# Kernel tuning notes

Measured on AMD Instinct MI355X. Metric: run time of the kernel, lower is better.

## Reference

```python
import jax, jax.numpy as jnp
import numpy as np

B, N, M = 4, 8192, 8192


def setup_inputs() -> dict:
    key = jax.random.key(0)
    k1, k2, k3, k4 = jax.random.split(key, 4)
    xyz1 = jax.random.normal(k1, (B, N, 3), dtype=jnp.float32)
    xyz2 = jax.random.normal(k2, (B, M, 3), dtype=jnp.float32)
    weights1 = jax.random.uniform(k3, (B, N), dtype=jnp.float32)
    weights2 = jax.random.uniform(k4, (B, M), dtype=jnp.float32)
    return {"xyz1": xyz1, "xyz2": xyz2, "weights1": weights1, "weights2": weights2}


def _chamfer_dists(xyz1, xyz2):
    # Squared L2 pairwise distances via the ||a||^2 + ||b||^2 - 2 a.b identity
    # (avoids materializing a [B, N, M, 3] difference tensor).
    sq1 = jnp.sum(xyz1 * xyz1, axis=-1)            # [B, N]
    sq2 = jnp.sum(xyz2 * xyz2, axis=-1)            # [B, M]
    dots = jnp.einsum("bnc,bmc->bnm", xyz1, xyz2)  # [B, N, M]
    d = sq1[:, :, None] + sq2[:, None, :] - 2.0 * dots
    d = jnp.maximum(d, 0.0)
    dist1 = jnp.min(d, axis=2)  # [B, N] nearest in xyz2 for each point in xyz1
    dist2 = jnp.min(d, axis=1)  # [B, M] nearest in xyz1 for each point in xyz2
    return dist1, dist2


def reference(xyz1, xyz2, weights1, weights2):
    dist1, dist2 = _chamfer_dists(xyz1, xyz2)
    dist1 = dist1 * weights1
    dist2 = dist2 * weights2
    dist1_avg = jnp.sum(dist1) / jnp.sum(weights1)
    dist2_avg = jnp.sum(dist2) / jnp.sum(weights2)
    return (dist1_avg + dist2_avg) / 2.0
```

## Files before the change

kernel.cpp:

```cpp
#include <hip/hip_runtime.h>

#define TPB 256
constexpr int Bsz  = 4;
constexpr int Npts = 8192;
constexpr int Mpts = 8192;
constexpr int PTS  = Bsz * Npts;
constexpr int QT_PER_B = Npts / 16;
constexpr int CT_PER_B = Mpts / 16;
constexpr int RBLK = 64;

typedef __attribute__((ext_vector_type(8))) short short8;
typedef __attribute__((ext_vector_type(4))) float f32x4;

__device__ __forceinline__ float min3f(float a, float b, float c) {
    return fminf(fminf(a, b), c);
}

__device__ __forceinline__ unsigned short bfh(float v) {
    unsigned u = __float_as_uint(v);
    return (unsigned short)((u + 0x7fffu + ((u >> 16) & 1u)) >> 16);
}
__device__ __forceinline__ float b2f(unsigned short h) {
    return __uint_as_float(((unsigned)h) << 16);
}
__device__ __forceinline__ void split3(float v, unsigned short& h,
                                       unsigned short& m, unsigned short& l) {
    h = bfh(v); float fh = b2f(h);
    m = bfh(v - fh); float fm = b2f(m);
    l = bfh(v - fh - fm);
}

__device__ __forceinline__ unsigned short pickA(int o, unsigned short h,
                                                unsigned short m, unsigned short l) {
    return o < 3 ? h : (o < 5 ? m : l);
}
__device__ __forceinline__ unsigned short pickB(int o, unsigned short h,
                                                unsigned short m, unsigned short l) {
    return (o == 1 || o == 4) ? m : (o == 2 ? l : h);
}

__global__ void __launch_bounds__(TPB) prep_kernel(
    const float* __restrict__ xyz1, const float* __restrict__ xyz2,
    short* __restrict__ aQ, short* __restrict__ bC)
{
    int id   = blockIdx.x * TPB + threadIdx.x;
    int side = id >> 17;
    int tl   = id & 131071;
    int tile = tl >> 6, lane = tl & 63;
    int r = lane & 15, g = lane >> 4;

    const float* src = side ? xyz2 : xyz1;
    int p = tile * 16 + r;
    float x = src[p * 3 + 0], y = src[p * 3 + 1], z = src[p * 3 + 2];
    float n = fmaf(x, x, fmaf(y, y, z * z));
    float s = side ? 1.f : -2.f;

    unsigned short xh, xm, xl, yh, ym, yl, zh, zm, zl, nh, nm, nl;
    split3(s * x, xh, xm, xl);
    split3(s * y, yh, ym, yl);
    split3(s * z, zh, zm, zl);
    split3(n, nh, nm, nl);
    const unsigned short ONE = 0x3F80;

    short8 v;
#pragma unroll
    for (int j = 0; j < 8; ++j) {
        int k = g * 8 + j;
        unsigned short u = 0;
        if (k < 18) {
            int c = k / 6, o = k - 6 * c;
            unsigned short h = c == 0 ? xh : (c == 1 ? yh : zh);
            unsigned short m = c == 0 ? xm : (c == 1 ? ym : zm);
            unsigned short l = c == 0 ? xl : (c == 1 ? yl : zl);
            u = side ? pickB(o, h, m, l) : pickA(o, h, m, l);
        } else if (k < 21) {
            u = side ? ONE : (k == 18 ? nh : (k == 19 ? nm : nl));
        } else if (k < 24) {
            u = side ? (k == 21 ? nh : (k == 22 ? nm : nl)) : ONE;
        }
        v[j] = (short)u;
    }
    short8* dst = (short8*)(side ? bC : aQ);
    dst[tile * 64 + lane] = v;
}

__global__ void __launch_bounds__(TPB, 4) chamfer_mfma_kernel(
    const short* __restrict__ aQ, const short* __restrict__ bC,
    unsigned int* __restrict__ partials)
{
    int bid = blockIdx.x;
    int linear = (bid & 7) * 256 + (bid >> 3);
    int batch = linear >> 9;
    int rem = linear & 511;
    int qs = rem >> 4;
    int cs = rem & 15;
    int w = threadIdx.x >> 6, lane = threadIdx.x & 63;

    int qtile0 = batch * QT_PER_B + qs * 16 + w * 4;
    int ctile0 = batch * CT_PER_B + cs * 32;

    const short8* aT = (const short8*)aQ;
    const short8* bT = (const short8*)bC;

    __shared__ unsigned int colb[512];
    colb[threadIdx.x]       = 0x7f7fffffu;
    colb[threadIdx.x + 256] = 0x7f7fffffu;

    short8 afrag[4];
#pragma unroll
    for (int t = 0; t < 4; ++t) afrag[t] = aT[(qtile0 + t) * 64 + lane];

    const f32x4 inf4 = {3.4e38f, 3.4e38f, 3.4e38f, 3.4e38f};
    const f32x4 zero4 = {0.f, 0.f, 0.f, 0.f};
    f32x4 rowp[4];
#pragma unroll
    for (int t = 0; t < 4; ++t) rowp[t] = inf4;
    __syncthreads();

    short8 bcur = bT[(ctile0 + 0) * 64 + lane];
    unsigned int* mycol = &colb[lane & 15];

    for (int ct = 0; ct < 32; ++ct) {
        short8 bnext = bT[(ctile0 + ((ct + 1) & 31)) * 64 + lane];

        f32x4 d[4];
#pragma unroll
        for (int t = 0; t < 4; ++t)
            d[t] = __builtin_amdgcn_mfma_f32_16x16x32_bf16(afrag[t], bcur, zero4, 0, 0, 0);

#pragma unroll
        for (int t = 0; t < 4; ++t)
            rowp[t] = __builtin_elementwise_min(rowp[t], d[t]);

        float ca = min3f(d[0][0], d[0][1], d[0][2]);
        ca = min3f(ca, d[0][3], d[1][0]);
        ca = min3f(ca, d[1][1], d[1][2]);
        ca = fminf(ca, d[1][3]);
        float cb = min3f(d[2][0], d[2][1], d[2][2]);
        cb = min3f(cb, d[2][3], d[3][0]);
        cb = min3f(cb, d[3][1], d[3][2]);
        cb = fminf(cb, d[3][3]);
        atomicMin(mycol + ct * 16, __float_as_uint(fmaxf(fminf(ca, cb), 0.f)));

        bcur = bnext;
    }

#pragma unroll
    for (int t = 0; t < 4; ++t) {
#pragma unroll
        for (int i = 0; i < 4; ++i) {
            float v = rowp[t][i];
            v = fminf(v, __shfl_xor(v, 1));
            v = fminf(v, __shfl_xor(v, 2));
            v = fminf(v, __shfl_xor(v, 4));
            v = fminf(v, __shfl_xor(v, 8));
            if ((lane & 15) == 0) {
                int q = (qtile0 + t) * 16 + (lane >> 4) * 4 + i;
                atomicMin(&partials[q], __float_as_uint(fmaxf(v, 0.f)));
            }
        }
    }

    __syncthreads();
    int cbase = PTS + ctile0 * 16;
    atomicMin(&partials[cbase + threadIdx.x],       colb[threadIdx.x]);
    atomicMin(&partials[cbase + threadIdx.x + 256], colb[threadIdx.x + 256]);
}

__global__ void __launch_bounds__(TPB) reduce_kernel(
    const float* __restrict__ partials,
    const float* __restrict__ w1, const float* __restrict__ w2,
    float2* __restrict__ slots)
{
    int gid = blockIdx.x * TPB + threadIdx.x;
    int dir = gid >> 13;
    int idx = gid & 8191;
    const float4* d4 = (const float4*)(partials + (size_t)dir * PTS);
    const float4* w4 = (const float4*)(dir ? w2 : w1);
    float4 d = d4[idx], w = w4[idx];
    float c = d.x * w.x + d.y * w.y + d.z * w.z + d.w * w.w;
    float s = w.x + w.y + w.z + w.w;

    for (int off = 32; off; off >>= 1) {
        c += __shfl_down(c, off);
        s += __shfl_down(s, off);
    }
    __shared__ float sc[4], ss[4];
    int lane = threadIdx.x & 63, wid = threadIdx.x >> 6;
    if (lane == 0) { sc[wid] = c; ss[wid] = s; }
    __syncthreads();
    if (threadIdx.x == 0) {
        slots[blockIdx.x] =
            make_float2(sc[0] + sc[1] + sc[2] + sc[3],
                        ss[0] + ss[1] + ss[2] + ss[3]);
    }
}

__global__ void __launch_bounds__(64) final_kernel(
    const float2* __restrict__ slots, float* __restrict__ out)
{
    float2 v = slots[threadIdx.x];
    for (int off = 16; off; off >>= 1) {
        v.x += __shfl_down(v.x, off, 32);
        v.y += __shfl_down(v.y, off, 32);
    }
    float c1 = __shfl(v.x, 32), s1 = __shfl(v.y, 32);
    if (threadIdx.x == 0)
        out[0] = 0.5f * (v.x / v.y + c1 / s1);
}

extern "C" void kernel_launch(void* const* d_in, const int* in_sizes, int n_in,
                              void* d_out, int out_size, void* d_ws, size_t ws_size,
                              hipStream_t stream) {
    const float* xyz1 = (const float*)d_in[0];
    const float* xyz2 = (const float*)d_in[1];
    const float* w1   = (const float*)d_in[2];
    const float* w2   = (const float*)d_in[3];
    float* out = (float*)d_out;

    unsigned int* partials = (unsigned int*)d_ws;
    float2* slots = (float2*)((char*)d_ws + (size_t)2 * PTS * sizeof(unsigned int));
    short* aQ = (short*)((char*)d_ws + (1u << 20));
    short* bC = (short*)((char*)d_ws + (4u << 20));

    prep_kernel<<<1024, TPB, 0, stream>>>(xyz1, xyz2, aQ, bC);
    chamfer_mfma_kernel<<<2048, TPB, 0, stream>>>(aQ, bC, partials);
    reduce_kernel<<<RBLK, TPB, 0, stream>>>((const float*)partials, w1, w2, slots);
    final_kernel<<<1, 64, 0, stream>>>(slots, out);
}
```

Before: 112.3 us.

## Double column tile per block and issue MFMAs via inline asm

Each block now covers 64 column tiles instead of 32, halving the grid to 1024 blocks and the number of per-block row-min and column-min flushes to global atomics. The four MFMAs per iteration are emitted as one inline asm block followed by fixed s_nops, replacing the compiler intrinsic. The explicit software prefetch of the next B fragment is replaced by a 4x unrolled loop with direct loads. The intent is less atomic and launch overhead and tighter MFMA issue. The trade-off is fewer blocks for latency hiding, a larger LDS buffer, and hard-coded nops that may over-stall or fail to cover result latency.

```diff
diff --git a/kernel.cpp b/kernel.cpp
--- a/kernel.cpp
+++ b/kernel.cpp
@@ -14,6 +14,21 @@
 
 __device__ __forceinline__ float min3f(float a, float b, float c) {
     return fminf(fminf(a, b), c);
+}
+
+__device__ __forceinline__ void mfma4_bf16(const short8& a0, const short8& a1,
+                                           const short8& a2, const short8& a3,
+                                           const short8& b,
+                                           f32x4& d0, f32x4& d1,
+                                           f32x4& d2, f32x4& d3) {
+    asm("v_mfma_f32_16x16x32_bf16 %0, %4, %8, 0\n\t"
+        "v_mfma_f32_16x16x32_bf16 %1, %5, %8, 0\n\t"
+        "v_mfma_f32_16x16x32_bf16 %2, %6, %8, 0\n\t"
+        "v_mfma_f32_16x16x32_bf16 %3, %7, %8, 0\n\t"
+        "s_nop 7\n\t"
+        "s_nop 3"
+        : "=&v"(d0), "=&v"(d1), "=&v"(d2), "=&v"(d3)
+        : "v"(a0), "v"(a1), "v"(a2), "v"(a3), "v"(b));
 }
 
 __device__ __forceinline__ unsigned short bfh(float v) {
@@ -89,60 +104,58 @@
     unsigned int* __restrict__ partials)
 {
     int bid = blockIdx.x;
-    int linear = (bid & 7) * 256 + (bid >> 3);
-    int batch = linear >> 9;
-    int rem = linear & 511;
-    int qs = rem >> 4;
-    int cs = rem & 15;
+    int linear = (bid & 7) * 128 + (bid >> 3);
+    int batch = linear >> 8;
+    int rem = linear & 255;
+    int qs = rem >> 3;
+    int cs = rem & 7;
     int w = threadIdx.x >> 6, lane = threadIdx.x & 63;
 
     int qtile0 = batch * QT_PER_B + qs * 16 + w * 4;
-    int ctile0 = batch * CT_PER_B + cs * 32;
+    int ctile0 = batch * CT_PER_B + cs * 64;
 
     const short8* aT = (const short8*)aQ;
     const short8* bT = (const short8*)bC;
 
-    __shared__ unsigned int colb[512];
-    colb[threadIdx.x]       = 0x7f7fffffu;
-    colb[threadIdx.x + 256] = 0x7f7fffffu;
+    __shared__ unsigned int colb[1024];
+#pragma unroll
+    for (int i = 0; i < 4; ++i)
+        colb[threadIdx.x + i * 256] = 0x7f7fffffu;
 
     short8 afrag[4];
 #pragma unroll
     for (int t = 0; t < 4; ++t) afrag[t] = aT[(qtile0 + t) * 64 + lane];
 
     const f32x4 inf4 = {3.4e38f, 3.4e38f, 3.4e38f, 3.4e38f};
-    const f32x4 zero4 = {0.f, 0.f, 0.f, 0.f};
     f32x4 rowp[4];
 #pragma unroll
     for (int t = 0; t < 4; ++t) rowp[t] = inf4;
     __syncthreads();
 
-    short8 bcur = bT[(ctile0 + 0) * 64 + lane];
+    const short8* bP = bT + ctile0 * 64 + lane;
     unsigned int* mycol = &colb[lane & 15];
 
-    for (int ct = 0; ct < 32; ++ct) {
-        short8 bnext = bT[(ctile0 + ((ct + 1) & 31)) * 64 + lane];
-
-        f32x4 d[4];
-#pragma unroll
-        for (int t = 0; t < 4; ++t)
-            d[t] = __builtin_amdgcn_mfma_f32_16x16x32_bf16(afrag[t], bcur, zero4, 0, 0, 0);
-
-#pragma unroll
-        for (int t = 0; t < 4; ++t)
-            rowp[t] = __builtin_elementwise_min(rowp[t], d[t]);
-
-        float ca = min3f(d[0][0], d[0][1], d[0][2]);
-        ca = min3f(ca, d[0][3], d[1][0]);
-        ca = min3f(ca, d[1][1], d[1][2]);
-        ca = fminf(ca, d[1][3]);
-        float cb = min3f(d[2][0], d[2][1], d[2][2]);
-        cb = min3f(cb, d[2][3], d[3][0]);
-        cb = min3f(cb, d[3][1], d[3][2]);
-        cb = fminf(cb, d[3][3]);
+#pragma unroll 4
+    for (int ct = 0; ct < 64; ++ct) {
+        short8 bf = bP[ct * 64];
+
+        f32x4 d0, d1, d2, d3;
+        mfma4_bf16(afrag[0], afrag[1], afrag[2], afrag[3], bf, d0, d1, d2, d3);
+
+        rowp[0] = __builtin_elementwise_min(rowp[0], d0);
+        rowp[1] = __builtin_elementwise_min(rowp[1], d1);
+        rowp[2] = __builtin_elementwise_min(rowp[2], d2);
+        rowp[3] = __builtin_elementwise_min(rowp[3], d3);
+
+        float ca = min3f(d0[0], d0[1], d0[2]);
+        ca = min3f(ca, d0[3], d1[0]);
+        ca = min3f(ca, d1[1], d1[2]);
+        ca = fminf(ca, d1[3]);
+        float cb = min3f(d2[0], d2[1], d2[2]);
+        cb = min3f(cb, d2[3], d3[0]);
+        cb = min3f(cb, d3[1], d3[2]);
+        cb = fminf(cb, d3[3]);
         atomicMin(mycol + ct * 16, __float_as_uint(fmaxf(fminf(ca, cb), 0.f)));
-
-        bcur = bnext;
     }
 
 #pragma unroll
@@ -163,8 +176,10 @@
 
     __syncthreads();
     int cbase = PTS + ctile0 * 16;
-    atomicMin(&partials[cbase + threadIdx.x],       colb[threadIdx.x]);
-    atomicMin(&partials[cbase + threadIdx.x + 256], colb[threadIdx.x + 256]);
+#pragma unroll
+    for (int i = 0; i < 4; ++i)
+        atomicMin(&partials[cbase + threadIdx.x + i * 256],
+                  colb[threadIdx.x + i * 256]);
 }
 
 __global__ void __launch_bounds__(TPB) reduce_kernel(
@@ -224,7 +239,7 @@
     short* bC = (short*)((char*)d_ws + (4u << 20));
 
     prep_kernel<<<1024, TPB, 0, stream>>>(xyz1, xyz2, aQ, bC);
-    chamfer_mfma_kernel<<<2048, TPB, 0, stream>>>(aQ, bC, partials);
+    chamfer_mfma_kernel<<<1024, TPB, 0, stream>>>(aQ, bC, partials);
     reduce_kernel<<<RBLK, TPB, 0, stream>>>((const float*)partials, w1, w2, slots);
     final_kernel<<<1, 64, 0, stream>>>(slots, out);
 }
```

Measured after the change: 105.2 us. 1.07x faster.
